# Optimization experiments

Measured on AMD Instinct MI355X. Metric: run time of the kernel, lower is better.

Reference implementation:

```python
import jax, jax.numpy as jnp
import numpy as np

B, T, F = 512, 98, 40
DIM, DEPTH, HEADS, DHEAD, MLP, NCLS = 192, 12, 3, 64, 768, 35
INNER = HEADS * DHEAD  # 192
N = T + 1  # cls token prepended
EPS = 1e-5


def _ln(x, g, b):
    m = jnp.mean(x, axis=-1, keepdims=True)
    v = jnp.mean(jnp.square(x - m), axis=-1, keepdims=True)
    return (x - m) * jax.lax.rsqrt(v + EPS) * g + b


def setup_inputs() -> dict:
    key = jax.random.key(0)
    ks = jax.random.split(key, 16)
    s = 0.02
    inp = {
        "img": jax.random.normal(ks[0], (B, T, F), jnp.float32),
        "lin_w": jax.random.normal(ks[1], (F, DIM), jnp.float32) * s,
        "g_feat": jax.random.normal(ks[2], (1, 1, DIM), jnp.float32),
        "pos_emb": jax.random.normal(ks[3], (1, N, DIM), jnp.float32),
        "ln1_g": jnp.ones((DEPTH, DIM), jnp.float32),
        "ln1_b": jnp.zeros((DEPTH, DIM), jnp.float32),
        "ln2_g": jnp.ones((DEPTH, DIM), jnp.float32),
        "ln2_b": jnp.zeros((DEPTH, DIM), jnp.float32),
        "qkv_w": jax.random.normal(ks[4], (DEPTH, DIM, 3 * INNER), jnp.float32) * s,
        "out_w": jax.random.normal(ks[5], (DEPTH, INNER, DIM), jnp.float32) * s,
        "out_b": jnp.zeros((DEPTH, DIM), jnp.float32),
        "ff1_w": jax.random.normal(ks[6], (DEPTH, DIM, MLP), jnp.float32) * s,
        "ff1_b": jnp.zeros((DEPTH, MLP), jnp.float32),
        "ff2_w": jax.random.normal(ks[7], (DEPTH, MLP, DIM), jnp.float32) * s,
        "ff2_b": jnp.zeros((DEPTH, DIM), jnp.float32),
        "head_ln_g": jnp.ones((DIM,), jnp.float32),
        "head_ln_b": jnp.zeros((DIM,), jnp.float32),
        "head_w": jax.random.normal(ks[8], (DIM, NCLS), jnp.float32) * s,
        "head_b": jnp.zeros((NCLS,), jnp.float32),
    }
    return inp


def reference(img, lin_w, g_feat, pos_emb, ln1_g, ln1_b, ln2_g, ln2_b,
              qkv_w, out_w, out_b, ff1_w, ff1_b, ff2_w, ff2_b,
              head_ln_g, head_ln_b, head_w, head_b):
    scale = DHEAD ** -0.5
    x = img @ lin_w  # [B, T, DIM]
    cls = jnp.broadcast_to(g_feat, (B, 1, DIM))
    x = jnp.concatenate([cls, x], axis=1) + pos_emb  # [B, N, DIM]

    for i in range(DEPTH):
        # --- attention (manual softmax, post-norm residual) ---
        qkv = x @ qkv_w[i]  # [B, N, 3*INNER]
        q, k, v = jnp.split(qkv, 3, axis=-1)
        rs = lambda t: t.reshape(B, N, HEADS, DHEAD).transpose(0, 2, 1, 3)
        q, k, v = rs(q), rs(k), rs(v)  # [B, H, N, D]
        dots = jnp.einsum('bhid,bhjd->bhij', q, k) * scale
        attn = jax.nn.softmax(dots, axis=-1)
        o = jnp.einsum('bhij,bhjd->bhid', attn, v)
        o = o.transpose(0, 2, 1, 3).reshape(B, N, INNER)
        o = o @ out_w[i] + out_b[i]
        x = _ln(o + x, ln1_g[i], ln1_b[i])
        # --- feedforward (exact GELU) ---
        h = jax.nn.gelu(x @ ff1_w[i] + ff1_b[i], approximate=False)
        f = h @ ff2_w[i] + ff2_b[i]
        x = _ln(f + x, ln2_g[i], ln2_b[i])

    x = x[:, 0]  # cls pooling
    x = _ln(x, head_ln_g, head_ln_b)
    return x @ head_w + head_b  # [B, NCLS]
```

## Files before the change

### kernel.cpp

```cpp
#include <hip/hip_runtime.h>

typedef unsigned short u16;

#define DIMM   192
#define DEPTH  12
#define NHEAD  3
#define MLPD   768
#define NCLS   35
#define NTOK   99
#define TIMG   98
#define FIMG   40
#define NBATCH 512
#define MT     7

#define XS_S 200
#define QH_S 72
#define VT_S 136
#define P_S  136
#define XS0  0
#define QH0  22400
#define KH0  30464
#define VT0  38528
#define P0   47232
#define RR_BYTE 124928
#define SMEM_BYTES 128512

typedef __attribute__((ext_vector_type(8))) __bf16 bf8;
typedef __attribute__((ext_vector_type(4))) float  f4;
typedef __attribute__((ext_vector_type(2))) unsigned u32x2;

__device__ __forceinline__ float b2f(u16 u){
  union { float f; unsigned u; } v; v.u = ((unsigned)u) << 16; return v.f;
}
__device__ __forceinline__ u16 f2b(float f){
  __bf16 h = (__bf16)f;
  union { __bf16 h; u16 u; } v; v.h = h;
  return v.u;
}
__device__ __forceinline__ u32x2 pack4(f4 a){
  u32x2 p;
  p.x = (unsigned)f2b(a[0]) | ((unsigned)f2b(a[1]) << 16);
  p.y = (unsigned)f2b(a[2]) | ((unsigned)f2b(a[3]) << 16);
  return p;
}
__device__ __forceinline__ f4 mm(bf8 a, bf8 b, f4 c){
  return __builtin_amdgcn_mfma_f32_16x16x32_bf16(a, b, c, 0, 0, 0);
}
__device__ __forceinline__ float gelu_f(float x){
  float z = x * 0.7071067811865476f;
  float az = fabsf(z);
  float t = 1.0f / (1.0f + 0.3275911f * az);
  float poly = ((((1.061405429f*t - 1.453152027f)*t + 1.421413741f)*t
                 - 0.284496736f)*t + 0.254829592f)*t;
  float erfv = 1.0f - poly * __expf(-az*az);
  erfv = (z < 0.0f) ? -erfv : erfv;
  return 0.5f * x * (1.0f + erfv);
}

extern "C" __global__ void permw(const float* __restrict__ src, u16* __restrict__ dst,
                                 int total, int KT, int NT, int realK, int Ndim){
  int i = blockIdx.x * 256 + threadIdx.x;
  if (i >= total) return;
  int j = i & 7, l = (i >> 3) & 63;
  int rest = i >> 9;
  int kt = rest % KT; rest /= KT;
  int nt = rest % NT; int layer = rest / NT;
  int k = kt*32 + (l>>4)*8 + j;
  int n = nt*16 + (l&15);
  float v = (k < realK) ? src[((size_t)layer*realK + k)*Ndim + n] : 0.0f;
  union { float f; unsigned u; } w; w.f = v;
  unsigned r = w.u + 0x7FFFu + ((w.u >> 16) & 1u);
  dst[i] = (u16)(r >> 16);
}

extern "C" __global__
__attribute__((amdgpu_flat_work_group_size(768,768), amdgpu_waves_per_eu(3,3)))
void vit_main(
    const float* __restrict__ img,   const float* __restrict__ g_feat,
    const float* __restrict__ pos_emb,
    const float* __restrict__ ln1_g, const float* __restrict__ ln1_b,
    const float* __restrict__ ln2_g, const float* __restrict__ ln2_b,
    const float* __restrict__ out_b, const float* __restrict__ ff1_b,
    const float* __restrict__ ff2_b,
    const float* __restrict__ hln_g, const float* __restrict__ hln_b,
    const float* __restrict__ head_w, const float* __restrict__ head_b,
    const u16* __restrict__ wlin, const u16* __restrict__ wqkv,
    const u16* __restrict__ wout, const u16* __restrict__ wff1,
    const u16* __restrict__ wff2,
    float* __restrict__ out)
{
  extern __shared__ __align__(16) u16 sm[];
  float* rowred = (float*)((char*)sm + RR_BYTE);
  const int tid  = threadIdx.x;
  const int lane = tid & 63;
  const int wv   = tid >> 6;
  const int wm   = wv >> 2;
  const int wn   = wv & 3;
  const int lg   = lane >> 4;
  const int lr   = lane & 15;
  const int b    = blockIdx.x;

  u16* const pA  = sm + XS0 + (wm*48 + lr)*XS_S + lg*8;
  u16* const pH  = sm + QH0 + (wm*48 + lr)*XS_S + lg*8;
  u16* const pOA = sm + QH0 + (wm*48 + lr)*QH_S + lg*8;
  u16* const pQS = sm + QH0 + (wm*48 + lr)*QH_S + wn*16 + lg*4;
  u16* const pVS = sm + VT0 + (wn*16 + lr)*VT_S + wm*48 + lg*4;
  u16* const pQA = sm + QH0 + (wv*16 + lr)*QH_S + lg*8;
  u16* const pKB = sm + KH0 + lr*QH_S + lg*8;
  u16* const pPS = sm + P0  + (wv*16 + lg*4)*P_S + lr;
  u16* const pPA = sm + P0  + (wv*16 + lr)*P_S + lg*8;
  u16* const pVB = sm + VT0 + lr*VT_S + lg*8;
  u16* const pOS = sm + QH0 + (wv*16 + lr)*QH_S + lg*4;
  u16* const pHS = sm + QH0 + (wm*48 + lr)*XS_S + wn*48 + lg*4;
  u16* const pXE = sm + XS0 + (wm*48 + lg*4)*XS_S + wn*48 + lr;
  float* const pRR = rowred + (wm*48 + lg*4)*8;
  float* const pRS = pRR + wn*2;

  for (int i = tid; i < SMEM_BYTES/4; i += 768) ((unsigned*)sm)[i] = 0u;
  __syncthreads();

  const f4 zero4 = {0.f,0.f,0.f,0.f};

  auto epilogue_ln = [&](f4 (&acc)[3][3],
                         const float* gptr, const float* bptr, const float* biasptr){
    float gg[3], bb[3], ob[3];
#pragma unroll
    for (int nt = 0; nt < 3; ++nt) {
      int c = wn*48 + nt*16 + lr;
      gg[nt] = gptr[c]; bb[nt] = bptr[c]; ob[nt] = biasptr[c];
    }
#pragma unroll
    for (int mi = 0; mi < 3; ++mi) {
      if (wm < 2 || mi == 0) {
#pragma unroll
        for (int r = 0; r < 4; ++r) {
          int ro = mi*16 + r;
          float s1 = 0.f, s2 = 0.f;
#pragma unroll
          for (int nt = 0; nt < 3; ++nt) {
            float v = acc[mi][nt][r] + ob[nt] + b2f(pXE[ro*XS_S + nt*16]);
            acc[mi][nt][r] = v;
            s1 += v; s2 += v*v;
          }
          s1 += __shfl_xor(s1,1); s2 += __shfl_xor(s2,1);
          s1 += __shfl_xor(s1,2); s2 += __shfl_xor(s2,2);
          s1 += __shfl_xor(s1,4); s2 += __shfl_xor(s2,4);
          s1 += __shfl_xor(s1,8); s2 += __shfl_xor(s2,8);
          if (lr == 0) {
            pRS[ro*8 + 0] = s1;
            pRS[ro*8 + 1] = s2;
          }
        }
      }
    }
    __syncthreads();
#pragma unroll
    for (int mi = 0; mi < 3; ++mi) {
      if (wm < 2 || mi == 0) {
#pragma unroll
        for (int r = 0; r < 4; ++r) {
          int ro = mi*16 + r;
          float4 q0 = *(const float4*)&pRR[ro*8];
          float4 q1 = *(const float4*)&pRR[ro*8 + 4];
          float S1 = q0.x + q0.z + q1.x + q1.z;
          float S2 = q0.y + q0.w + q1.y + q1.w;
          float mean = S1 * (1.0f/DIMM);
          float var  = S2 * (1.0f/DIMM) - mean*mean;
          float rs = rsqrtf(var + 1e-5f);
          int row = wm*48 + ro + lg*4;
          if (row < NTOK) {
#pragma unroll
            for (int nt = 0; nt < 3; ++nt) {
              float y = (acc[mi][nt][r] - mean)*rs*gg[nt] + bb[nt];
              pXE[ro*XS_S + nt*16] = f2b(y);
            }
          }
        }
      }
    }
    __syncthreads();
  };

  const float* imgb = img + (size_t)b * (TIMG*FIMG);
  for (int i = tid; i < TIMG*FIMG; i += 768) {
    int r = i / FIMG, c = i - r*FIMG;
    sm[QH0 + (r+1)*QH_S + c] = f2b(imgb[i]);
  }
  __syncthreads();
  {
    const u16* wl = wlin + (size_t)(wn*3)*2*512 + lane*8;
    bf8 Bf[3][2];
#pragma unroll
    for (int nt = 0; nt < 3; ++nt)
#pragma unroll
      for (int kt = 0; kt < 2; ++kt)
        Bf[nt][kt] = *(const bf8*)&wl[(nt*2+kt)*512];
#pragma unroll
    for (int mi = 0; mi < 3; ++mi) {
      if (wm < 2 || mi == 0) {
        bf8 Af[2];
#pragma unroll
        for (int kt = 0; kt < 2; ++kt)
          Af[kt] = *(const bf8*)&pOA[mi*16*QH_S + kt*32];
#pragma unroll
        for (int nt = 0; nt < 3; ++nt) {
          f4 a = zero4;
#pragma unroll
          for (int kt = 0; kt < 2; ++kt) a = mm(Af[kt], Bf[nt][kt], a);
          int col = wn*48 + nt*16 + lr;
#pragma unroll
          for (int r = 0; r < 4; ++r) {
            int row = wm*48 + mi*16 + lg*4 + r;
            if (row < NTOK) {
              float v = a[r] + pos_emb[row*DIMM + col] + (row==0 ? g_feat[col] : 0.f);
              pXE[(mi*16+r)*XS_S + nt*16] = f2b(v);
            }
          }
        }
      }
    }
  }
  __syncthreads();

  for (int L = 0; L < DEPTH; ++L) {
    const u16* wq = wqkv + (size_t)L*36*6*512;
    f4 oacc[3][3];
#pragma unroll
    for (int mi = 0; mi < 3; ++mi)
#pragma unroll
      for (int nt = 0; nt < 3; ++nt) oacc[mi][nt] = zero4;

    for (int h = 0; h < NHEAD; ++h) {
      {
        const u16* wp = wq + ((size_t)(h*4 + wn)*6)*512 + lane*8;
        bf8 B[6];
#pragma unroll
        for (int kt = 0; kt < 6; ++kt) B[kt] = *(const bf8*)&wp[kt*512];
#pragma unroll
        for (int mi = 0; mi < 3; ++mi) {
          if (wm < 2 || mi == 0) {
            bf8 Af[6];
#pragma unroll
            for (int kt = 0; kt < 6; ++kt)
              Af[kt] = *(const bf8*)&pA[mi*16*XS_S + kt*32];
            f4 a = zero4;
#pragma unroll
            for (int kt = 0; kt < 6; ++kt) a = mm(B[kt], Af[kt], a);
            a = a * 0.125f;
            *(u32x2*)(pQS + mi*16*QH_S) = pack4(a);
          }
        }
      }
      {
        const u16* wp = wq + ((size_t)(12 + h*4 + wn)*6)*512 + lane*8;
        bf8 B[6];
#pragma unroll
        for (int kt = 0; kt < 6; ++kt) B[kt] = *(const bf8*)&wp[kt*512];
#pragma unroll
        for (int mi = 0; mi < 3; ++mi) {
          if (wm < 2 || mi == 0) {
            bf8 Af[6];
#pragma unroll
            for (int kt = 0; kt < 6; ++kt)
              Af[kt] = *(const bf8*)&pA[mi*16*XS_S + kt*32];
            f4 a = zero4;
#pragma unroll
            for (int kt = 0; kt < 6; ++kt) a = mm(B[kt], Af[kt], a);
            *(u32x2*)(pQS + (KH0-QH0) + mi*16*QH_S) = pack4(a);
          }
        }
      }
      {
        const u16* wp = wq + ((size_t)(24 + h*4 + wn)*6)*512 + lane*8;
        bf8 B[6];
#pragma unroll
        for (int kt = 0; kt < 6; ++kt) B[kt] = *(const bf8*)&wp[kt*512];
#pragma unroll
        for (int mi = 0; mi < 3; ++mi) {
          if (wm < 2 || mi == 0) {
            bf8 Af[6];
#pragma unroll
            for (int kt = 0; kt < 6; ++kt)
              Af[kt] = *(const bf8*)&pA[mi*16*XS_S + kt*32];
            f4 a = zero4;
#pragma unroll
            for (int kt = 0; kt < 6; ++kt) a = mm(Af[kt], B[kt], a);
            *(u32x2*)(pVS + mi*16) = pack4(a);
          }
        }
      }
      __syncthreads();

      if (wv < MT) {
        bf8 Aq[2];
#pragma unroll
        for (int ks = 0; ks < 2; ++ks)
          Aq[ks] = *(const bf8*)&pQA[ks*32];
        f4 s[7];
#pragma unroll
        for (int kt = 0; kt < 7; ++kt) {
          f4 a = zero4;
#pragma unroll
          for (int ks = 0; ks < 2; ++ks) {
            bf8 Bk2 = *(const bf8*)&pKB[kt*16*QH_S + ks*32];
            a = mm(Aq[ks], Bk2, a);
          }
          s[kt] = a;
        }
#pragma unroll
        for (int r = 0; r < 4; ++r) {
          float m = s[0][r];
#pragma unroll
          for (int kt = 1; kt < 6; ++kt) m = fmaxf(m, s[kt][r]);
          m = fmaxf(m, (lr < 3) ? s[6][r] : -1e30f);
          m = fmaxf(m, __shfl_xor(m, 1));
          m = fmaxf(m, __shfl_xor(m, 2));
          m = fmaxf(m, __shfl_xor(m, 4));
          m = fmaxf(m, __shfl_xor(m, 8));
          float p[7]; float sum = 0.f;
#pragma unroll
          for (int kt = 0; kt < 6; ++kt) { p[kt] = __expf(s[kt][r] - m); sum += p[kt]; }
          p[6] = (lr < 3) ? __expf(s[6][r] - m) : 0.f;
          sum += p[6];
          sum += __shfl_xor(sum, 1);
          sum += __shfl_xor(sum, 2);
          sum += __shfl_xor(sum, 4);
          sum += __shfl_xor(sum, 8);
          float inv = 1.0f / sum;
#pragma unroll
          for (int kt = 0; kt < 7; ++kt)
            pPS[r*P_S + kt*16] = f2b(p[kt]*inv);
        }
        asm volatile("" ::: "memory");
        bf8 Ap[4];
#pragma unroll
        for (int ks = 0; ks < 4; ++ks)
          Ap[ks] = *(const bf8*)&pPA[ks*32];
#pragma unroll
        for (int nt = 0; nt < 4; ++nt) {
          f4 a = zero4;
#pragma unroll
          for (int ks = 0; ks < 4; ++ks) {
            bf8 Bv2 = *(const bf8*)&pVB[nt*16*VT_S + ks*32];
            a = mm(Bv2, Ap[ks], a);
          }
          *(u32x2*)(pOS + nt*16) = pack4(a);
        }
      }
      __syncthreads();

      {
        const u16* wp = wout + (((size_t)(L*12 + wn*3)*6) + h*2)*512 + lane*8;
        bf8 Bo[3][2];
#pragma unroll
        for (int nt = 0; nt < 3; ++nt)
#pragma unroll
          for (int ks = 0; ks < 2; ++ks)
            Bo[nt][ks] = *(const bf8*)&wp[(nt*6 + ks)*512];
#pragma unroll
        for (int mi = 0; mi < 3; ++mi) {
          if (wm < 2 || mi == 0) {
            bf8 Ao[2];
#pragma unroll
            for (int ks = 0; ks < 2; ++ks)
              Ao[ks] = *(const bf8*)&pOA[mi*16*QH_S + ks*32];
#pragma unroll
            for (int nt = 0; nt < 3; ++nt)
#pragma unroll
              for (int ks = 0; ks < 2; ++ks)
                oacc[mi][nt] = mm(Ao[ks], Bo[nt][ks], oacc[mi][nt]);
          }
        }
      }
      __syncthreads();
    }

    epilogue_ln(oacc, ln1_g + L*DIMM, ln1_b + L*DIMM, out_b + L*DIMM);

    f4 facc[3][3];
#pragma unroll
    for (int mi = 0; mi < 3; ++mi)
#pragma unroll
      for (int nt = 0; nt < 3; ++nt) facc[mi][nt] = zero4;

    for (int blk = 0; blk < 4; ++blk) {
      {
        const u16* wp = wff1 + ((size_t)(L*48 + blk*12 + wn*3)*6)*512 + lane*8;
        const float* fbp = ff1_b + L*MLPD + blk*192 + wn*48;
#pragma unroll
        for (int nt = 0; nt < 3; ++nt) {
          bf8 B[6];
#pragma unroll
          for (int kt = 0; kt < 6; ++kt) B[kt] = *(const bf8*)&wp[(nt*6+kt)*512];
          float4 fb4 = *(const float4*)&fbp[nt*16 + lg*4];
#pragma unroll
          for (int mi = 0; mi < 3; ++mi) {
            if (wm < 2 || mi == 0) {
              bf8 Af[6];
#pragma unroll
              for (int kt = 0; kt < 6; ++kt)
                Af[kt] = *(const bf8*)&pA[mi*16*XS_S + kt*32];
              f4 a = zero4;
#pragma unroll
              for (int kt = 0; kt < 6; ++kt) a = mm(B[kt], Af[kt], a);
              f4 g;
              g[0] = gelu_f(a[0] + fb4.x);
              g[1] = gelu_f(a[1] + fb4.y);
              g[2] = gelu_f(a[2] + fb4.z);
              g[3] = gelu_f(a[3] + fb4.w);
              *(u32x2*)(pHS + mi*16*XS_S + nt*16) = pack4(g);
            }
          }
        }
      }
      __syncthreads();
      {
        const u16* wp = wff2 + ((size_t)(L*12 + wn*3)*24 + blk*6)*512 + lane*8;
#pragma unroll
        for (int nt = 0; nt < 3; ++nt) {
          bf8 B[6];
#pragma unroll
          for (int kt = 0; kt < 6; ++kt) B[kt] = *(const bf8*)&wp[(nt*24+kt)*512];
#pragma unroll
          for (int mi = 0; mi < 3; ++mi) {
            if (wm < 2 || mi == 0) {
              bf8 Ah[6];
#pragma unroll
              for (int kt = 0; kt < 6; ++kt)
                Ah[kt] = *(const bf8*)&pH[mi*16*XS_S + kt*32];
#pragma unroll
              for (int kt = 0; kt < 6; ++kt)
                facc[mi][nt] = mm(Ah[kt], B[kt], facc[mi][nt]);
            }
          }
        }
      }
      __syncthreads();
    }

    epilogue_ln(facc, ln2_g + L*DIMM, ln2_b + L*DIMM, ff2_b + L*DIMM);
  }

  float* yv = rowred;
  if (wv == 0) {
    float x0 = b2f(sm[XS0 + lane]);
    float x1 = b2f(sm[XS0 + 64 + lane]);
    float x2 = b2f(sm[XS0 + 128 + lane]);
    float s1 = x0+x1+x2;
    float s2 = x0*x0 + x1*x1 + x2*x2;
#pragma unroll
    for (int d = 1; d < 64; d <<= 1) { s1 += __shfl_xor(s1, d); s2 += __shfl_xor(s2, d); }
    float mean = s1*(1.0f/DIMM), var = s2*(1.0f/DIMM) - mean*mean;
    float rs = rsqrtf(var + 1e-5f);
    yv[lane]      = (x0-mean)*rs*hln_g[lane]      + hln_b[lane];
    yv[64+lane]   = (x1-mean)*rs*hln_g[64+lane]   + hln_b[64+lane];
    yv[128+lane]  = (x2-mean)*rs*hln_g[128+lane]  + hln_b[128+lane];
  }
  __syncthreads();
  if (tid < NCLS) {
    float acc = head_b[tid];
    for (int k = 0; k < DIMM; ++k) acc += yv[k] * head_w[k*NCLS + tid];
    out[(size_t)b*NCLS + tid] = acc;
  }
}

extern "C" void kernel_launch(void* const* d_in, const int* in_sizes, int n_in,
                              void* d_out, int out_size, void* d_ws, size_t ws_size,
                              hipStream_t stream) {
  const float* img    = (const float*)d_in[0];
  const float* lin_w  = (const float*)d_in[1];
  const float* g_feat = (const float*)d_in[2];
  const float* pos_emb= (const float*)d_in[3];
  const float* ln1_g  = (const float*)d_in[4];
  const float* ln1_b  = (const float*)d_in[5];
  const float* ln2_g  = (const float*)d_in[6];
  const float* ln2_b  = (const float*)d_in[7];
  const float* qkv_w  = (const float*)d_in[8];
  const float* out_w  = (const float*)d_in[9];
  const float* out_b  = (const float*)d_in[10];
  const float* ff1_w  = (const float*)d_in[11];
  const float* ff1_b  = (const float*)d_in[12];
  const float* ff2_w  = (const float*)d_in[13];
  const float* ff2_b  = (const float*)d_in[14];
  const float* hln_g  = (const float*)d_in[15];
  const float* hln_b  = (const float*)d_in[16];
  const float* head_w = (const float*)d_in[17];
  const float* head_b = (const float*)d_in[18];

  u16* ws   = (u16*)d_ws;
  u16* wlin = ws;
  u16* wqkv = wlin + 12288;
  u16* wout = wqkv + 1327104;
  u16* wff1 = wout + 442368;
  u16* wff2 = wff1 + 1769472;

  struct PermArgs { const float* src; u16* dst; int layers, Kdim, Ndim, realK; };
  const PermArgs pa[5] = {
    { lin_w, wlin, 1, 64, 192, 40 },
    { qkv_w, wqkv, 12, 192, 576, 192 },
    { out_w, wout, 12, 192, 192, 192 },
    { ff1_w, wff1, 12, 192, 768, 192 },
    { ff2_w, wff2, 12, 768, 192, 768 },
  };
  for (int i = 0; i < 5; ++i) {
    int total = pa[i].layers * (pa[i].Ndim/16) * (pa[i].Kdim/32) * 512;
    hipLaunchKernelGGL(permw, dim3((total + 255)/256), dim3(256), 0, stream,
                       pa[i].src, pa[i].dst, total, pa[i].Kdim/32, pa[i].Ndim/16,
                       pa[i].realK, pa[i].Ndim);
  }

  hipFuncSetAttribute(reinterpret_cast<const void*>(vit_main),
                      hipFuncAttributeMaxDynamicSharedMemorySize, SMEM_BYTES);

  hipLaunchKernelGGL(vit_main, dim3(NBATCH), dim3(768), SMEM_BYTES, stream,
                     img, g_feat, pos_emb, ln1_g, ln1_b, ln2_g, ln2_b,
                     out_b, ff1_b, ff2_b, hln_g, hln_b, head_w, head_b,
                     wlin, wqkv, wout, wff1, wff2, (float*)d_out);
}
```

Baseline: 1.521 ms.

## Transpose MFMA outputs so softmax and LayerNorm reduce in-lane with vector stores

Swaps the MFMA operand order for the QK^T, out-projection and FF2 products so that each lane holds four consecutive columns of one row instead of four rows. This lets softmax and the LayerNorm epilogue reduce mostly inside the lane plus two cross-lane shuffles instead of four, and write bf16 results as packed 8-byte stores instead of scalar 2-byte stores. It also folds log2(e) into the Q scale so softmax can use exp2f. The cost is a different row-sum layout in shared memory and vector loads of gamma, beta and bias, with a small change in rounding.

```diff
diff --git a/kernel.cpp b/kernel.cpp
--- a/kernel.cpp
+++ b/kernel.cpp
@@ -25,12 +25,20 @@
 #define RR_BYTE 124928
 #define SMEM_BYTES 128512
 
+#define QSCALE 0.1803368801111243f
+
 typedef __attribute__((ext_vector_type(8))) __bf16 bf8;
 typedef __attribute__((ext_vector_type(4))) float  f4;
 typedef __attribute__((ext_vector_type(2))) unsigned u32x2;
 
 __device__ __forceinline__ float b2f(u16 u){
   union { float f; unsigned u; } v; v.u = ((unsigned)u) << 16; return v.f;
+}
+__device__ __forceinline__ float blo(unsigned u){
+  union { float f; unsigned u; } v; v.u = u << 16; return v.f;
+}
+__device__ __forceinline__ float bhi(unsigned u){
+  union { float f; unsigned u; } v; v.u = u & 0xffff0000u; return v.f;
 }
 __device__ __forceinline__ u16 f2b(float f){
   __bf16 h = (__bf16)f;
@@ -107,14 +115,13 @@
   u16* const pVS = sm + VT0 + (wn*16 + lr)*VT_S + wm*48 + lg*4;
   u16* const pQA = sm + QH0 + (wv*16 + lr)*QH_S + lg*8;
   u16* const pKB = sm + KH0 + lr*QH_S + lg*8;
-  u16* const pPS = sm + P0  + (wv*16 + lg*4)*P_S + lr;
+  u16* const pPT = sm + P0  + (wv*16 + lr)*P_S + lg*4;
   u16* const pPA = sm + P0  + (wv*16 + lr)*P_S + lg*8;
   u16* const pVB = sm + VT0 + lr*VT_S + lg*8;
   u16* const pOS = sm + QH0 + (wv*16 + lr)*QH_S + lg*4;
   u16* const pHS = sm + QH0 + (wm*48 + lr)*XS_S + wn*48 + lg*4;
+  u16* const pXT = sm + XS0 + (wm*48 + lr)*XS_S + wn*48 + lg*4;
   u16* const pXE = sm + XS0 + (wm*48 + lg*4)*XS_S + wn*48 + lr;
-  float* const pRR = rowred + (wm*48 + lg*4)*8;
-  float* const pRS = pRR + wn*2;
 
   for (int i = tid; i < SMEM_BYTES/4; i += 768) ((unsigned*)sm)[i] = 0u;
   __syncthreads();
@@ -123,33 +130,36 @@
 
   auto epilogue_ln = [&](f4 (&acc)[3][3],
                          const float* gptr, const float* bptr, const float* biasptr){
-    float gg[3], bb[3], ob[3];
+    float4 g4[3], b4[3], ob4[3];
 #pragma unroll
     for (int nt = 0; nt < 3; ++nt) {
-      int c = wn*48 + nt*16 + lr;
-      gg[nt] = gptr[c]; bb[nt] = bptr[c]; ob[nt] = biasptr[c];
+      int c = wn*48 + nt*16 + lg*4;
+      g4[nt]  = *(const float4*)&gptr[c];
+      b4[nt]  = *(const float4*)&bptr[c];
+      ob4[nt] = *(const float4*)&biasptr[c];
     }
 #pragma unroll
     for (int mi = 0; mi < 3; ++mi) {
       if (wm < 2 || mi == 0) {
-#pragma unroll
-        for (int r = 0; r < 4; ++r) {
-          int ro = mi*16 + r;
-          float s1 = 0.f, s2 = 0.f;
-#pragma unroll
-          for (int nt = 0; nt < 3; ++nt) {
-            float v = acc[mi][nt][r] + ob[nt] + b2f(pXE[ro*XS_S + nt*16]);
-            acc[mi][nt][r] = v;
-            s1 += v; s2 += v*v;
-          }
-          s1 += __shfl_xor(s1,1); s2 += __shfl_xor(s2,1);
-          s1 += __shfl_xor(s1,2); s2 += __shfl_xor(s2,2);
-          s1 += __shfl_xor(s1,4); s2 += __shfl_xor(s2,4);
-          s1 += __shfl_xor(s1,8); s2 += __shfl_xor(s2,8);
-          if (lr == 0) {
-            pRS[ro*8 + 0] = s1;
-            pRS[ro*8 + 1] = s2;
-          }
+        const int row = wm*48 + mi*16 + lr;
+        float s1 = 0.f, s2 = 0.f;
+#pragma unroll
+        for (int nt = 0; nt < 3; ++nt) {
+          u32x2 xo = *(const u32x2*)(pXT + mi*16*XS_S + nt*16);
+          float v0 = acc[mi][nt][0] + ob4[nt].x + blo(xo.x);
+          float v1 = acc[mi][nt][1] + ob4[nt].y + bhi(xo.x);
+          float v2 = acc[mi][nt][2] + ob4[nt].z + blo(xo.y);
+          float v3 = acc[mi][nt][3] + ob4[nt].w + bhi(xo.y);
+          acc[mi][nt][0] = v0; acc[mi][nt][1] = v1;
+          acc[mi][nt][2] = v2; acc[mi][nt][3] = v3;
+          s1 += (v0+v1)+(v2+v3);
+          s2 += v0*v0; s2 += v1*v1; s2 += v2*v2; s2 += v3*v3;
+        }
+        s1 += __shfl_xor(s1,16); s2 += __shfl_xor(s2,16);
+        s1 += __shfl_xor(s1,32); s2 += __shfl_xor(s2,32);
+        if (lg == 0) {
+          float2 pr; pr.x = s1; pr.y = s2;
+          *(float2*)&rowred[row*8 + wn*2] = pr;
         }
       }
     }
@@ -157,23 +167,23 @@
 #pragma unroll
     for (int mi = 0; mi < 3; ++mi) {
       if (wm < 2 || mi == 0) {
-#pragma unroll
-        for (int r = 0; r < 4; ++r) {
-          int ro = mi*16 + r;
-          float4 q0 = *(const float4*)&pRR[ro*8];
-          float4 q1 = *(const float4*)&pRR[ro*8 + 4];
-          float S1 = q0.x + q0.z + q1.x + q1.z;
-          float S2 = q0.y + q0.w + q1.y + q1.w;
-          float mean = S1 * (1.0f/DIMM);
-          float var  = S2 * (1.0f/DIMM) - mean*mean;
-          float rs = rsqrtf(var + 1e-5f);
-          int row = wm*48 + ro + lg*4;
-          if (row < NTOK) {
-#pragma unroll
-            for (int nt = 0; nt < 3; ++nt) {
-              float y = (acc[mi][nt][r] - mean)*rs*gg[nt] + bb[nt];
-              pXE[ro*XS_S + nt*16] = f2b(y);
-            }
+        const int row = wm*48 + mi*16 + lr;
+        float4 q0 = *(const float4*)&rowred[row*8];
+        float4 q1 = *(const float4*)&rowred[row*8 + 4];
+        float S1 = (q0.x + q0.z) + (q1.x + q1.z);
+        float S2 = (q0.y + q0.w) + (q1.y + q1.w);
+        float mean = S1 * (1.0f/DIMM);
+        float var  = S2 * (1.0f/DIMM) - mean*mean;
+        float rs = rsqrtf(var + 1e-5f);
+        if (row < NTOK) {
+#pragma unroll
+          for (int nt = 0; nt < 3; ++nt) {
+            f4 y;
+            y[0] = (acc[mi][nt][0]-mean)*rs*g4[nt].x + b4[nt].x;
+            y[1] = (acc[mi][nt][1]-mean)*rs*g4[nt].y + b4[nt].y;
+            y[2] = (acc[mi][nt][2]-mean)*rs*g4[nt].z + b4[nt].z;
+            y[3] = (acc[mi][nt][3]-mean)*rs*g4[nt].w + b4[nt].w;
+            *(u32x2*)(pXT + mi*16*XS_S + nt*16) = pack4(y);
           }
         }
       }
@@ -246,7 +256,7 @@
             f4 a = zero4;
 #pragma unroll
             for (int kt = 0; kt < 6; ++kt) a = mm(B[kt], Af[kt], a);
-            a = a * 0.125f;
+            a = a * QSCALE;
             *(u32x2*)(pQS + mi*16*QH_S) = pack4(a);
           }
         }
@@ -296,40 +306,44 @@
 #pragma unroll
         for (int ks = 0; ks < 2; ++ks)
           Aq[ks] = *(const bf8*)&pQA[ks*32];
-        f4 s[7];
+        f4 sT[7];
 #pragma unroll
         for (int kt = 0; kt < 7; ++kt) {
           f4 a = zero4;
 #pragma unroll
           for (int ks = 0; ks < 2; ++ks) {
             bf8 Bk2 = *(const bf8*)&pKB[kt*16*QH_S + ks*32];
-            a = mm(Aq[ks], Bk2, a);
-          }
-          s[kt] = a;
-        }
+            a = mm(Bk2, Aq[ks], a);
+          }
+          sT[kt] = a;
+        }
+        float m = -1e30f;
+#pragma unroll
+        for (int kt = 0; kt < 6; ++kt)
+#pragma unroll
+          for (int r = 0; r < 4; ++r) m = fmaxf(m, sT[kt][r]);
+        if (lg == 0) { m = fmaxf(m, fmaxf(sT[6][0], fmaxf(sT[6][1], sT[6][2]))); }
+        m = fmaxf(m, __shfl_xor(m, 16));
+        m = fmaxf(m, __shfl_xor(m, 32));
+        float pT[7][4]; float sum = 0.f;
+#pragma unroll
+        for (int kt = 0; kt < 6; ++kt)
+#pragma unroll
+          for (int r = 0; r < 4; ++r) { float p = exp2f(sT[kt][r] - m); pT[kt][r] = p; sum += p; }
 #pragma unroll
         for (int r = 0; r < 4; ++r) {
-          float m = s[0][r];
-#pragma unroll
-          for (int kt = 1; kt < 6; ++kt) m = fmaxf(m, s[kt][r]);
-          m = fmaxf(m, (lr < 3) ? s[6][r] : -1e30f);
-          m = fmaxf(m, __shfl_xor(m, 1));
-          m = fmaxf(m, __shfl_xor(m, 2));
-          m = fmaxf(m, __shfl_xor(m, 4));
-          m = fmaxf(m, __shfl_xor(m, 8));
-          float p[7]; float sum = 0.f;
-#pragma unroll
-          for (int kt = 0; kt < 6; ++kt) { p[kt] = __expf(s[kt][r] - m); sum += p[kt]; }
-          p[6] = (lr < 3) ? __expf(s[6][r] - m) : 0.f;
-          sum += p[6];
-          sum += __shfl_xor(sum, 1);
-          sum += __shfl_xor(sum, 2);
-          sum += __shfl_xor(sum, 4);
-          sum += __shfl_xor(sum, 8);
-          float inv = 1.0f / sum;
-#pragma unroll
-          for (int kt = 0; kt < 7; ++kt)
-            pPS[r*P_S + kt*16] = f2b(p[kt]*inv);
+          float p = (lg == 0 && r < 3) ? exp2f(sT[6][r] - m) : 0.f;
+          pT[6][r] = p; sum += p;
+        }
+        sum += __shfl_xor(sum, 16);
+        sum += __shfl_xor(sum, 32);
+        float inv = 1.0f / sum;
+#pragma unroll
+        for (int kt = 0; kt < 7; ++kt) {
+          f4 pp;
+          pp[0] = pT[kt][0]*inv; pp[1] = pT[kt][1]*inv;
+          pp[2] = pT[kt][2]*inv; pp[3] = pT[kt][3]*inv;
+          *(u32x2*)(pPT + kt*16) = pack4(pp);
         }
         asm volatile("" ::: "memory");
         bf8 Ap[4];
@@ -368,7 +382,7 @@
             for (int nt = 0; nt < 3; ++nt)
 #pragma unroll
               for (int ks = 0; ks < 2; ++ks)
-                oacc[mi][nt] = mm(Ao[ks], Bo[nt][ks], oacc[mi][nt]);
+                oacc[mi][nt] = mm(Bo[nt][ks], Ao[ks], oacc[mi][nt]);
           }
         }
       }
@@ -430,7 +444,7 @@
                 Ah[kt] = *(const bf8*)&pH[mi*16*XS_S + kt*32];
 #pragma unroll
               for (int kt = 0; kt < 6; ++kt)
-                facc[mi][nt] = mm(Ah[kt], B[kt], facc[mi][nt]);
+                facc[mi][nt] = mm(B[kt], Ah[kt], facc[mi][nt]);
             }
           }
         }
```

After: 1.372 ms. 1.11x faster.
